# Kernel optimization log

Hardware: AMD Instinct MI355X
Metric: run time of the kernel (lower is better)

The kernel has to match this reference:

```python
import jax, jax.numpy as jnp
import numpy as np

B, T, D, H, L = 64, 256, 64, 512, 10


def setup_inputs() -> dict:
    key = jax.random.key(0)
    ks = jax.random.split(key, 8)
    k_init = 1.0 / np.sqrt(H)  # PyTorch LSTMCell/Linear uniform init bound
    u = lambda k, shape: jax.random.uniform(k, shape, jnp.float32, -k_init, k_init)
    return {
        "x": jax.random.normal(ks[0], (B, T, D), jnp.float32),
        "W_ih0": u(ks[1], (4 * H, D)),        # layer 0 input weights
        "W_ih": u(ks[2], (L - 1, 4 * H, H)),  # layers 1..L-1 input weights
        "W_hh": u(ks[3], (L, 4 * H, H)),      # recurrent weights
        "b_ih": u(ks[4], (L, 4 * H)),
        "b_hh": u(ks[5], (L, 4 * H)),
        "W_out": u(ks[6], (D, H)),            # linear head weight
        "b_out": u(ks[7], (D,)),
    }


def _cell(x, h, c, W_i, W_h, b):
    # PyTorch LSTMCell: gates ordered (i, f, g, o)
    g = x @ W_i.T + h @ W_h.T + b  # [B, 4H]
    i, f, gg, o = jnp.split(g, 4, axis=-1)
    i = jax.nn.sigmoid(i)
    f = jax.nn.sigmoid(f)
    o = jax.nn.sigmoid(o)
    gg = jnp.tanh(gg)
    c_new = f * c + i * gg
    h_new = o * jnp.tanh(c_new)
    return h_new, c_new


def reference(x, W_ih0, W_ih, W_hh, b_ih, b_hh, W_out, b_out):
    b = b_ih + b_hh  # [L, 4H] — biases only ever appear summed

    def step(carry, x_t):
        h, c = carry  # each [L, B, H]
        h0, c0 = _cell(x_t, h[0], c[0], W_ih0, W_hh[0], b[0])
        hs, cs = [h0], [c0]
        for i in range(1, L):  # fixed small layer count
            hi, ci = _cell(hs[-1], h[i], c[i], W_ih[i - 1], W_hh[i], b[i])
            hs.append(hi)
            cs.append(ci)
        y = hs[-1] @ W_out.T + b_out  # [B, D] per-step linear head
        return (jnp.stack(hs), jnp.stack(cs)), y

    init = (jnp.zeros((L, B, H), jnp.float32), jnp.zeros((L, B, H), jnp.float32))
    _, ys = jax.lax.scan(step, init, jnp.swapaxes(x, 0, 1))  # ys: [T, B, D]
    return jnp.swapaxes(ys, 0, 1)  # [B, T, D]
```

## Files before the change

kernel.cpp:

```cpp
#include <hip/hip_runtime.h>
#include <hip/hip_fp16.h>
#include <stdint.h>

typedef _Float16 h8 __attribute__((ext_vector_type(8)));
typedef float f4 __attribute__((ext_vector_type(4)));

#define MFMA16(a,b,c) __builtin_amdgcn_mfma_f32_16x16x32_f16((a),(b),(c),0,0,0)

constexpr size_t XT_OFF = 0;
constexpr size_t XT_BYTES = 256ull * 4096 * 2;
constexpr size_t HL_OFF = XT_OFF + XT_BYTES;
constexpr size_t HL_BYTES = 10ull * 8 * 65536;
constexpr size_t HX_OFF = HL_OFF + HL_BYTES;
constexpr size_t HX_BYTES = 5ull * 8 * 65536;
constexpr size_t WSTRM_OFF = HX_OFF + HX_BYTES;
constexpr size_t WSTRM_BYTES = 144ull * 106496;
constexpr size_t PX_OFF = WSTRM_OFF + WSTRM_BYTES;
constexpr size_t CNT_OFF = PX_OFF + 1024;
constexpr size_t DIAG_OFF = CNT_OFF + 64;
constexpr size_t WS_NEED = DIAG_OFF + 64;

#define SCR 155648

__device__ __forceinline__ const char* unif(const void* p) {
  uint64_t u = (uint64_t)p;
  uint32_t lo = __builtin_amdgcn_readfirstlane((uint32_t)u);
  uint32_t hi = __builtin_amdgcn_readfirstlane((uint32_t)(u >> 32));
  return (const char*)(((uint64_t)hi << 32) | lo);
}

__device__ __forceinline__ h8 gld16_p(const void* base, int voff) {
  h8 v; asm volatile("global_load_dwordx4 %0, %1, %2" : "=v"(v) : "v"(voff), "s"(base)); return v;
}
__device__ __forceinline__ h8 gld16_sc1(const void* base, int voff) {
  h8 v; asm volatile("global_load_dwordx4 %0, %1, %2 sc1" : "=v"(v) : "v"(voff), "s"(base)); return v;
}
__device__ __forceinline__ void gst16_sc1(const void* base, int voff, h8 v) {
  asm volatile("global_store_dwordx4 %0, %1, %2 sc1" :: "v"(voff), "v"(v), "s"(base) : "memory");
}
#define WAITI(n) do { asm volatile("s_waitcnt vmcnt(" #n ")" ::: "memory"); \
                      __builtin_amdgcn_sched_barrier(0); } while (0)

__device__ __forceinline__ int ld_prog(const int* p) {
  return __hip_atomic_load(p, __ATOMIC_RELAXED, __HIP_MEMORY_SCOPE_AGENT);
}
__device__ __forceinline__ void st_prog(int* p, int v) {
  __hip_atomic_store(p, v, __ATOMIC_RELAXED, __HIP_MEMORY_SCOPE_AGENT);
  __builtin_amdgcn_sched_barrier(0);
}
#define INV_L1() asm volatile("buffer_inv sc0\n\ts_waitcnt vmcnt(0)" ::: "memory")

__device__ __forceinline__ float sigm(float x) { return __fdividef(1.f, 1.f + __expf(-x)); }
__device__ __forceinline__ float tanh_f(float x) { return 1.f - __fdividef(2.f, __expf(2.f*x) + 1.f); }

__global__ __launch_bounds__(256) void zero_kernel(char* ws) {
  int i = blockIdx.x * 256 + threadIdx.x;
  if (i < 163840) {
    int layer = i >> 14, w = i & 16383;
    ((int*)(ws + HL_OFF))[(size_t)layer * 8 * 16384 + w] = 0;
  } else {
    int j = i - 163840;
    if (j < 168) ((int*)(ws + PX_OFF))[j] = -1;
    else if (j < 176) ((int*)(ws + CNT_OFF))[j - 168] = 0;
    else if (j == 176) ((int*)(ws + DIAG_OFF))[0] = 0;
  }
}

__global__ __launch_bounds__(256) void xprep_kernel(const float* __restrict__ X, char* ws) {
  int u = blockIdx.x * 256 + threadIdx.x;
  if (u >= 131072) return;
  int t = u >> 9, rem = u & 511, kg = rem >> 6, b = rem & 63;
  const float* src = X + ((size_t)b * 256 + t) * 64 + kg * 8;
  h8 v;
#pragma unroll
  for (int j = 0; j < 8; ++j) v[j] = (_Float16)src[j];
  *(h8*)(ws + XT_OFF + (size_t)u * 16) = v;
}

__global__ __launch_bounds__(256) void wsprep_kernel(const float* __restrict__ Wih,
                                                     const float* __restrict__ Whh, char* ws) {
  int u = blockIdx.x * 256 + threadIdx.x;
  if (u >= 144 * 6656) return;
  int cu = u / 6656, rem = u % 6656;
  int s = rem / 512, rem2 = rem % 512;
  int nt = rem2 >> 6, l = rem2 & 63;
  int ppc = l >> 2, lgc = l & 3;
  int L = 1 + cu / 16, cl = cu % 16, hbase = cl * 32;
  int kt = 4 + s, k = kt * 32 + lgc * 8;
  int row = (nt & 3) * 512 + hbase + ((nt >> 2) << 4) + ppc;
  const float* src = (k < 512) ? (Wih + (size_t)(L - 1) * 1048576 + (size_t)row * 512 + k)
                               : (Whh + (size_t)L * 1048576 + (size_t)row * 512 + (k - 512));
  h8 v;
#pragma unroll
  for (int j = 0; j < 8; ++j) v[j] = (_Float16)src[j];
  uint32_t off = (uint32_t)(ppc * 64 + lgc * 16) ^ (uint32_t)((ppc & 7) << 4);
  *(h8*)(ws + WSTRM_OFF + (size_t)cu * 106496 + (size_t)s * 8192 + (size_t)nt * 1024 + off) = v;
}

#define KTRES(r, Areg) do {                                                     \
  _Pragma("unroll") for (int nt_ = 0; nt_ < 8; ++nt_) {                         \
    h8 bv_ = *(const h8*)(lds + ((((r) * 8 + nt_) << 10) + swzo));              \
    acc[nt_] = MFMA16((Areg), bv_, acc[nt_]); } } while (0)

#define KTSTR(s, Areg) do {                                                     \
  _Pragma("unroll") for (int nt_ = 0; nt_ < 8; ++nt_)                           \
    acc[nt_] = MFMA16((Areg), Bst[s][nt_], acc[nt_]); } while (0)

#define ISSB(s) do { _Pragma("unroll") for (int nt_ = 0; nt_ < 8; ++nt_)        \
    Bst[s][nt_] = gld16_p(strm, (s) * 8192 + (nt_ << 10) + (int)swzo); } while (0)

#define ISSAS(i0) do { _Pragma("unroll") for (int i_ = 0; i_ < 4; ++i_)         \
    AS[(i0) + i_] = gld16_p(selb, ((i0) + i_) * 4096 + abb); } while (0)

__global__ __launch_bounds__(256, 1) void lstm_fused(
    const float* __restrict__ X, const float* __restrict__ Wih0,
    const float* __restrict__ Wih, const float* __restrict__ Whh,
    const float* __restrict__ bih, const float* __restrict__ bhh,
    const float* __restrict__ Wout, const float* __restrict__ bout,
    float* __restrict__ out, char* __restrict__ ws)
{
  extern __shared__ char lds[];
  const int tid = threadIdx.x;
  const int lane = tid & 63;
  const int wv = tid >> 6;
  const int pp = lane & 15;
  const int lg = lane >> 4;
  const int abb = lg * 1024 + (16 * wv + pp) * 16;
  const uint32_t swzo = (uint32_t)(pp * 64 + lg * 16) ^ (uint32_t)((pp & 7) << 4);

  int* progX = (int*)(ws + PX_OFF);
  int* diag  = (int*)(ws + DIAG_OFF);
  const char* hl = ws + HL_OFF;
  const char* hx = ws + HX_OFF;

  int xcd;
  asm volatile("s_getreg_b32 %0, hwreg(HW_REG_XCC_ID)" : "=s"(xcd));
  xcd &= 7;
  if (tid == 0) {
    int s = atomicAdd((int*)(ws + CNT_OFF) + xcd, 1);
    *(int*)lds = s;
  }
  __syncthreads();
  const int slot = __builtin_amdgcn_readfirstlane(*(int*)lds);
  __syncthreads();

  if (xcd == 5) {
    if (slot >= 8) return;
    const int hd = slot, d0 = hd * 8;
    const float* wrow0 = Wout + (size_t)(d0 + wv) * 512;
    const float* wrow1 = Wout + (size_t)(d0 + 4 + wv) * 512;
    const int b = lane;
    const bool pv = lane < 16;
    const int* pw = progX + 144 + (lane & 15);
    for (int th = 0; th < 256; ++th) {
      if (wv == 0) {
        int it = 0; bool bailed = false;
        for (;;) {
          int v = ld_prog(pw);
          if (__ballot(!pv || v >= th) == ~0ull) break;
          __builtin_amdgcn_s_sleep(1);
          if (++it > 60000) { bailed = true; break; }
        }
        if (bailed && lane == 0) atomicMax(diag, 10000 + th);
      }
      __builtin_amdgcn_s_barrier();
      const char* h9 = unif(hx + (size_t)(4 * 8 + ((th + 1) & 7)) * 65536);
      h8 H0[16], H1[16], H2[16], H3[16];
#pragma unroll
      for (int i = 0; i < 16; ++i) H0[i] = gld16_sc1(h9, i * 1024 + b * 16);
#pragma unroll
      for (int i = 0; i < 16; ++i) H1[i] = gld16_sc1(h9, (16 + i) * 1024 + b * 16);
      float a0 = bout[d0 + wv], a1 = bout[d0 + 4 + wv];
#define KH(kb, H) do { _Pragma("unroll") for (int i_ = 0; i_ < 16; ++i_) {      \
        h8 hv_ = H[i_]; float hf_[8];                                           \
        _Pragma("unroll") for (int j_ = 0; j_ < 8; ++j_) hf_[j_] = (float)hv_[j_]; \
        int kg_ = (kb) + i_;                                                    \
        f4 w0_ = *(const f4*)(wrow0 + kg_ * 8); f4 w1_ = *(const f4*)(wrow0 + kg_ * 8 + 4); \
        a0 += hf_[0]*w0_[0]+hf_[1]*w0_[1]+hf_[2]*w0_[2]+hf_[3]*w0_[3]           \
            + hf_[4]*w1_[0]+hf_[5]*w1_[1]+hf_[6]*w1_[2]+hf_[7]*w1_[3];          \
        f4 u0_ = *(const f4*)(wrow1 + kg_ * 8); f4 u1_ = *(const f4*)(wrow1 + kg_ * 8 + 4); \
        a1 += hf_[0]*u0_[0]+hf_[1]*u0_[1]+hf_[2]*u0_[2]+hf_[3]*u0_[3]           \
            + hf_[4]*u1_[0]+hf_[5]*u1_[1]+hf_[6]*u1_[2]+hf_[7]*u1_[3]; } } while (0)
      WAITI(16); KH(0, H0);
#pragma unroll
      for (int i = 0; i < 16; ++i) H2[i] = gld16_sc1(h9, (32 + i) * 1024 + b * 16);
      WAITI(16); KH(16, H1);
#pragma unroll
      for (int i = 0; i < 16; ++i) H3[i] = gld16_sc1(h9, (48 + i) * 1024 + b * 16);
      WAITI(16); KH(32, H2);
      WAITI(0);  KH(48, H3);
      out[(size_t)b * 16384 + (size_t)th * 64 + d0 + wv] = a0;
      out[(size_t)b * 16384 + (size_t)th * 64 + d0 + 4 + wv] = a1;
      __syncthreads();
      if (tid == 0) st_prog(progX + 160 + hd, th);
    }
    if (hd == 0 && tid == 0) {
      int dv = ld_prog(diag);
      if (dv != 0) out[0] = 1.0e6f + (float)dv;
    }
    return;
  }
  if (xcd > 5 || slot >= 32) return;

  const int L = 2 * xcd + (slot >= 16);
  const int cl = slot & 15;
  const int hbase = cl * 32;
  const bool oddL = (L & 1) != 0;

  if (L == 0) {
    for (int ch = tid; ch < 9216; ch += 256) {
      int r = ch >> 9, rem = ch & 511;
      int nt = rem >> 6, l = rem & 63, ppc = l >> 2, lgc = l & 3;
      int k = r * 32 + lgc * 8;
      int row = (nt & 3) * 512 + hbase + ((nt >> 2) << 4) + ppc;
      const float* src = (k < 64) ? (Wih0 + (size_t)row * 64 + k)
                                  : (Whh + (size_t)row * 512 + (k - 64));
      h8 v;
#pragma unroll
      for (int j = 0; j < 8; ++j) v[j] = (_Float16)src[j];
      uint32_t off = (uint32_t)(ppc * 64 + lgc * 16) ^ (uint32_t)((ppc & 7) << 4);
      *(h8*)(lds + ((r * 8 + nt) << 10) + off) = v;
    }
  } else {
    const float* WihL = Wih + (size_t)(L - 1) * 1048576;
    const float* WhhL = Whh + (size_t)L * 1048576;
    for (int ch = tid; ch < 9728; ch += 256) {
      int r = ch >> 9, rem = ch & 511;
      int nt = rem >> 6, l = rem & 63, ppc = l >> 2, lgc = l & 3;
      int rkt = r < 4 ? r : r + 13;
      int k = rkt * 32 + lgc * 8;
      int row = (nt & 3) * 512 + hbase + ((nt >> 2) << 4) + ppc;
      const float* src = (k < 512) ? (WihL + (size_t)row * 512 + k)
                                   : (WhhL + (size_t)row * 512 + (k - 512));
      h8 v;
#pragma unroll
      for (int j = 0; j < 8; ++j) v[j] = (_Float16)src[j];
      uint32_t off = (uint32_t)(ppc * 64 + lgc * 16) ^ (uint32_t)((ppc & 7) << 4);
      *(h8*)(lds + ((r * 8 + nt) << 10) + off) = v;
    }
  }
  float biasv[8];
#pragma unroll
  for (int nt = 0; nt < 8; ++nt) {
    int row = (nt & 3) * 512 + hbase + ((nt >> 2) << 4) + pp;
    biasv[nt] = bih[L * 2048 + row] + bhh[L * 2048 + row];
  }
  __syncthreads();

  const int jl = lane & 15;
  const int* pw = progX; bool pv = false; int dlt = 0;
  if (lane < 16)      { pv = true; pw = progX + L * 16 + jl; dlt = -1; }
  else if (lane < 32) { if (L > 0) { pv = true; pw = progX + (L - 1) * 16 + jl; dlt = 0; } }
  else if (lane < 48) {
    dlt = -7;
    if (L == 9) { if (jl < 8) { pv = true; pw = progX + 160 + jl; } }
    else        { pv = true; pw = progX + (L + 1) * 16 + jl; }
  }

  const char* strm = unif(ws + WSTRM_OFF + (size_t)((L - 1) * 16 + cl) * 106496);
  const char* xt = ws + XT_OFF;

  float cv[2][4] = {{0,0,0,0},{0,0,0,0}};

  for (int t = 0; t < 256; ++t) {
    if (wv == 0) {
      int it = 0; bool bailed = false;
      for (;;) {
        int v = ld_prog(pw);
        if (__ballot(!pv || v >= t + dlt) == ~0ull) break;
        __builtin_amdgcn_s_sleep(1);
        if (++it > 60000) { bailed = true; break; }
      }
      if (bailed && lane == 0) atomicMax(diag, L * 1000 + t);
      INV_L1();
    }
    __builtin_amdgcn_s_barrier();

    f4 acc[8];
#pragma unroll
    for (int j = 0; j < 8; ++j) acc[j] = (f4){0.f, 0.f, 0.f, 0.f};

    if (L == 0) {
      const char* selb = unif(hl + (size_t)(t & 7) * 65536);
      const char* xtb = unif(xt + (size_t)t * 8192);
      h8 X0 = gld16_p(xtb, abb);
      h8 X1 = gld16_p(xtb, 4096 + abb);
      h8 AS[16];
#pragma unroll
      for (int i = 0; i < 16; ++i) AS[i] = gld16_p(selb, i * 4096 + abb);
      WAITI(17); KTRES(0, X0);
      WAITI(16); KTRES(1, X1);
      WAITI(15); KTRES(2, AS[0]);  WAITI(14); KTRES(3, AS[1]);
      WAITI(13); KTRES(4, AS[2]);  WAITI(12); KTRES(5, AS[3]);
      WAITI(11); KTRES(6, AS[4]);  WAITI(10); KTRES(7, AS[5]);
      WAITI(9);  KTRES(8, AS[6]);  WAITI(8);  KTRES(9, AS[7]);
      WAITI(7);  KTRES(10, AS[8]); WAITI(6);  KTRES(11, AS[9]);
      WAITI(5);  KTRES(12, AS[10]); WAITI(4); KTRES(13, AS[11]);
      WAITI(3);  KTRES(14, AS[12]); WAITI(2); KTRES(15, AS[13]);
      WAITI(1);  KTRES(16, AS[14]); WAITI(0); KTRES(17, AS[15]);
    } else {
      const char* botb = unif(oddL
          ? (hl + (size_t)((L - 1) * 8 + ((t + 1) & 7)) * 65536)
          : (hx + (size_t)(((L - 1) >> 1) * 8 + ((t + 1) & 7)) * 65536));
      const char* selb = unif(hl + (size_t)(L * 8 + (t & 7)) * 65536);
      h8 AB[16], AS[16], Bst[13][8];
      if (oddL) {
#pragma unroll
        for (int i = 0; i < 16; ++i) AB[i] = gld16_p(botb, i * 4096 + abb);
      } else {
#pragma unroll
        for (int i = 0; i < 16; ++i) AB[i] = gld16_sc1(botb, i * 4096 + abb);
      }
      ISSB(0); ISSB(1);
      WAITI(31); KTRES(0, AB[0]); ISSB(2);
      WAITI(38); KTRES(1, AB[1]); ISSB(3);
      WAITI(45); KTRES(2, AB[2]); ISSB(4);
      WAITI(52); KTRES(3, AB[3]); ISSB(5);
      WAITI(40); KTSTR(0, AB[4]); ISSB(6);
      WAITI(40); KTSTR(1, AB[5]); ISSB(7);
      WAITI(40); KTSTR(2, AB[6]); ISSB(8);
      WAITI(40); KTSTR(3, AB[7]); ISSB(9);
      WAITI(40); KTSTR(4, AB[8]); ISSB(10);
      WAITI(40); KTSTR(5, AB[9]); ISSB(11);
      WAITI(40); KTSTR(6, AB[10]); ISSB(12);
      WAITI(40); KTSTR(7, AB[11]); ISSAS(0);
      WAITI(36); KTSTR(8, AB[12]); ISSAS(4);
      WAITI(28); KTSTR(9, AB[13]); ISSAS(8);
      WAITI(20); KTSTR(10, AB[14]); ISSAS(12);
      WAITI(12); KTSTR(11, AB[15]);
      WAITI(4);  KTSTR(12, AS[0]);
      KTRES(4, AS[1]);  KTRES(5, AS[2]);  KTRES(6, AS[3]);
      KTRES(7, AS[4]);  KTRES(8, AS[5]);  KTRES(9, AS[6]);
      KTRES(10, AS[7]); KTRES(11, AS[8]); KTRES(12, AS[9]);
      KTRES(13, AS[10]); KTRES(14, AS[11]);
      WAITI(3); KTRES(15, AS[12]);
      WAITI(2); KTRES(16, AS[13]);
      WAITI(1); KTRES(17, AS[14]);
      WAITI(0); KTRES(18, AS[15]);
    }

    const int brow = 16 * wv + 4 * lg;
#pragma unroll
    for (int jh = 0; jh < 2; ++jh) {
      const int hgl = jh * 16 + pp;
#pragma unroll
      for (int r = 0; r < 4; ++r) {
        float gi = sigm(acc[4*jh+0][r] + biasv[4*jh+0]);
        float gf = sigm(acc[4*jh+1][r] + biasv[4*jh+1]);
        float gg = tanh_f(acc[4*jh+2][r] + biasv[4*jh+2]);
        float go = sigm(acc[4*jh+3][r] + biasv[4*jh+3]);
        float cc = gf * cv[jh][r] + gi * gg;
        cv[jh][r] = cc;
        float hh = go * tanh_f(cc);
        *(_Float16*)(lds + SCR + ((hgl >> 3) << 10) + (brow + r) * 16 + ((hgl & 7) << 1))
            = (_Float16)hh;
      }
    }
    __syncthreads();
    {
      const int kg_l = tid >> 6, b = tid & 63;
      h8 vv = *(const h8*)(lds + SCR + tid * 16);
      const int goff = (((hbase >> 3) + kg_l) << 10) + b * 16;
      const char* HdL = unif(hl + (size_t)(L * 8 + ((t + 1) & 7)) * 65536);
      asm volatile("global_store_dwordx4 %0, %1, %2" :: "v"(goff), "v"(vv), "s"(HdL) : "memory");
      if (oddL) {
        const char* HdX = unif(hx + (size_t)((L >> 1) * 8 + ((t + 1) & 7)) * 65536);
        gst16_sc1(HdX, goff, vv);
      }
    }
    asm volatile("s_waitcnt vmcnt(0)" ::: "memory");
    __syncthreads();
    if (tid == 0) st_prog(progX + L * 16 + cl, t);
  }
}

extern "C" void kernel_launch(void* const* d_in, const int* in_sizes, int n_in,
                              void* d_out, int out_size, void* d_ws, size_t ws_size,
                              hipStream_t stream) {
  const float* X    = (const float*)d_in[0];
  const float* Wih0 = (const float*)d_in[1];
  const float* Wih  = (const float*)d_in[2];
  const float* Whh  = (const float*)d_in[3];
  const float* bihp = (const float*)d_in[4];
  const float* bhhp = (const float*)d_in[5];
  const float* Wout = (const float*)d_in[6];
  const float* bout = (const float*)d_in[7];
  float* out = (float*)d_out;
  char* ws = (char*)d_ws;
  (void)in_sizes; (void)n_in; (void)out_size;
  if (ws_size < WS_NEED) return;

  hipFuncSetAttribute((const void*)lstm_fused,
                      hipFuncAttributeMaxDynamicSharedMemorySize, 163840);

  zero_kernel<<<642, 256, 0, stream>>>(ws);
  xprep_kernel<<<512, 256, 0, stream>>>(X, ws);
  wsprep_kernel<<<3744, 256, 0, stream>>>(Wih, Whh, ws);
  lstm_fused<<<256, 256, 163840, stream>>>(X, Wih0, Wih, Whh, bihp, bhhp,
                                           Wout, bout, out, ws);
}
```

Before: 2.912 ms.

## Double waves per block by splitting gate columns across wave pairs

Raises the block size from 256 to 512 threads. Each pair of waves now shares one batch row group and splits the 8 gate column tiles, four per wave, which halves the accumulators, streamed B registers and MFMA chain length per wave. The goal is more latency hiding and a shorter per-step critical path in the serial recurrence. In exchange, both waves of a pair load the same A fragments, block barriers now span more waves, and the vmcnt wait counts and layer-0 LDS indexing had to be retuned by hand.

New measurement: 5.882 ms. +102.0%, slower.

```diff
diff --git a/kernel.cpp b/kernel.cpp
--- a/kernel.cpp
+++ b/kernel.cpp
@@ -34,6 +34,9 @@
 }
 __device__ __forceinline__ h8 gld16_sc1(const void* base, int voff) {
   h8 v; asm volatile("global_load_dwordx4 %0, %1, %2 sc1" : "=v"(v) : "v"(voff), "s"(base)); return v;
+}
+__device__ __forceinline__ void gst16_p(const void* base, int voff, h8 v) {
+  asm volatile("global_store_dwordx4 %0, %1, %2" :: "v"(voff), "v"(v), "s"(base) : "memory");
 }
 __device__ __forceinline__ void gst16_sc1(const void* base, int voff, h8 v) {
   asm volatile("global_store_dwordx4 %0, %1, %2 sc1" :: "v"(voff), "v"(v), "s"(base) : "memory");
@@ -98,21 +101,29 @@
 }
 
 #define KTRES(r, Areg) do {                                                     \
-  _Pragma("unroll") for (int nt_ = 0; nt_ < 8; ++nt_) {                         \
-    h8 bv_ = *(const h8*)(lds + ((((r) * 8 + nt_) << 10) + swzo));              \
+  _Pragma("unroll") for (int nt_ = 0; nt_ < 4; ++nt_) {                         \
+    h8 bv_ = *(const h8*)(lds + ((((r) * 8 + c4 + nt_) << 10) + swzo));         \
     acc[nt_] = MFMA16((Areg), bv_, acc[nt_]); } } while (0)
 
 #define KTSTR(s, Areg) do {                                                     \
-  _Pragma("unroll") for (int nt_ = 0; nt_ < 8; ++nt_)                           \
+  _Pragma("unroll") for (int nt_ = 0; nt_ < 4; ++nt_)                           \
     acc[nt_] = MFMA16((Areg), Bst[s][nt_], acc[nt_]); } while (0)
 
-#define ISSB(s) do { _Pragma("unroll") for (int nt_ = 0; nt_ < 8; ++nt_)        \
-    Bst[s][nt_] = gld16_p(strm, (s) * 8192 + (nt_ << 10) + (int)swzo); } while (0)
+#define ISSB(s) do { _Pragma("unroll") for (int nt_ = 0; nt_ < 4; ++nt_)        \
+    Bst[s][nt_] = gld16_p(strm, (s) * 8192 + ((c4 + nt_) << 10) + (int)swzo); } while (0)
 
 #define ISSAS(i0) do { _Pragma("unroll") for (int i_ = 0; i_ < 4; ++i_)         \
     AS[(i0) + i_] = gld16_p(selb, ((i0) + i_) * 4096 + abb); } while (0)
 
-__global__ __launch_bounds__(256, 1) void lstm_fused(
+#define KB0(kt, Av) do {                                                        \
+  _Pragma("unroll") for (int jj_ = 0; jj_ < 4; ++jj_) {                         \
+    int c_ = 16 * (c4 + jj_) + pp;                                              \
+    uint32_t off_ = (uint32_t)(c_ * 1152 + (kt) * 64 + lg * 16)                 \
+                  ^ (uint32_t)((c_ & 7) << 4);                                  \
+    h8 bv_ = *(const h8*)(lds + off_);                                          \
+    acc[jj_] = MFMA16((Av), bv_, acc[jj_]); } } while (0)
+
+__global__ __launch_bounds__(512, 1) void lstm_fused(
     const float* __restrict__ X, const float* __restrict__ Wih0,
     const float* __restrict__ Wih, const float* __restrict__ Whh,
     const float* __restrict__ bih, const float* __restrict__ bhh,
@@ -123,9 +134,12 @@
   const int tid = threadIdx.x;
   const int lane = tid & 63;
   const int wv = tid >> 6;
+  const int g = wv >> 1;
+  const int cw = wv & 1;
+  const int c4 = cw << 2;
   const int pp = lane & 15;
   const int lg = lane >> 4;
-  const int abb = lg * 1024 + (16 * wv + pp) * 16;
+  const int abb = lg * 1024 + (16 * g + pp) * 16;
   const uint32_t swzo = (uint32_t)(pp * 64 + lg * 16) ^ (uint32_t)((pp & 7) << 4);
 
   int* progX = (int*)(ws + PX_OFF);
@@ -163,14 +177,15 @@
         }
         if (bailed && lane == 0) atomicMax(diag, 10000 + th);
       }
-      __builtin_amdgcn_s_barrier();
-      const char* h9 = unif(hx + (size_t)(4 * 8 + ((th + 1) & 7)) * 65536);
-      h8 H0[16], H1[16], H2[16], H3[16];
-#pragma unroll
-      for (int i = 0; i < 16; ++i) H0[i] = gld16_sc1(h9, i * 1024 + b * 16);
-#pragma unroll
-      for (int i = 0; i < 16; ++i) H1[i] = gld16_sc1(h9, (16 + i) * 1024 + b * 16);
-      float a0 = bout[d0 + wv], a1 = bout[d0 + 4 + wv];
+      __syncthreads();
+      if (wv < 4) {
+        const char* h9 = unif(hx + (size_t)(4 * 8 + ((th + 1) & 7)) * 65536);
+        h8 H0[16], H1[16], H2[16], H3[16];
+#pragma unroll
+        for (int i = 0; i < 16; ++i) H0[i] = gld16_sc1(h9, i * 1024 + b * 16);
+#pragma unroll
+        for (int i = 0; i < 16; ++i) H1[i] = gld16_sc1(h9, (16 + i) * 1024 + b * 16);
+        float a0 = bout[d0 + wv], a1 = bout[d0 + 4 + wv];
 #define KH(kb, H) do { _Pragma("unroll") for (int i_ = 0; i_ < 16; ++i_) {      \
         h8 hv_ = H[i_]; float hf_[8];                                           \
         _Pragma("unroll") for (int j_ = 0; j_ < 8; ++j_) hf_[j_] = (float)hv_[j_]; \
@@ -181,16 +196,17 @@
         f4 u0_ = *(const f4*)(wrow1 + kg_ * 8); f4 u1_ = *(const f4*)(wrow1 + kg_ * 8 + 4); \
         a1 += hf_[0]*u0_[0]+hf_[1]*u0_[1]+hf_[2]*u0_[2]+hf_[3]*u0_[3]           \
             + hf_[4]*u1_[0]+hf_[5]*u1_[1]+hf_[6]*u1_[2]+hf_[7]*u1_[3]; } } while (0)
-      WAITI(16); KH(0, H0);
-#pragma unroll
-      for (int i = 0; i < 16; ++i) H2[i] = gld16_sc1(h9, (32 + i) * 1024 + b * 16);
-      WAITI(16); KH(16, H1);
-#pragma unroll
-      for (int i = 0; i < 16; ++i) H3[i] = gld16_sc1(h9, (48 + i) * 1024 + b * 16);
-      WAITI(16); KH(32, H2);
-      WAITI(0);  KH(48, H3);
-      out[(size_t)b * 16384 + (size_t)th * 64 + d0 + wv] = a0;
-      out[(size_t)b * 16384 + (size_t)th * 64 + d0 + 4 + wv] = a1;
+        WAITI(16); KH(0, H0);
+#pragma unroll
+        for (int i = 0; i < 16; ++i) H2[i] = gld16_sc1(h9, (32 + i) * 1024 + b * 16);
+        WAITI(16); KH(16, H1);
+#pragma unroll
+        for (int i = 0; i < 16; ++i) H3[i] = gld16_sc1(h9, (48 + i) * 1024 + b * 16);
+        WAITI(16); KH(32, H2);
+        WAITI(0);  KH(48, H3);
+        out[(size_t)b * 16384 + (size_t)th * 64 + d0 + wv] = a0;
+        out[(size_t)b * 16384 + (size_t)th * 64 + d0 + 4 + wv] = a1;
+      }
       __syncthreads();
       if (tid == 0) st_prog(progX + 160 + hd, th);
     }
@@ -208,7 +224,7 @@
   const bool oddL = (L & 1) != 0;
 
   if (L == 0) {
-    for (int ch = tid; ch < 9216; ch += 256) {
+    for (int ch = tid; ch < 9216; ch += 512) {
       int r = ch >> 9, rem = ch & 511;
       int nt = rem >> 6, l = rem & 63, ppc = l >> 2, lgc = l & 3;
       int k = r * 32 + lgc * 8;
@@ -224,7 +240,7 @@
   } else {
     const float* WihL = Wih + (size_t)(L - 1) * 1048576;
     const float* WhhL = Whh + (size_t)L * 1048576;
-    for (int ch = tid; ch < 9728; ch += 256) {
+    for (int ch = tid; ch < 9728; ch += 512) {
       int r = ch >> 9, rem = ch & 511;
       int nt = rem >> 6, l = rem & 63, ppc = l >> 2, lgc = l & 3;
       int rkt = r < 4 ? r : r + 13;
@@ -239,11 +255,11 @@
       *(h8*)(lds + ((r * 8 + nt) << 10) + off) = v;
     }
   }
-  float biasv[8];
-#pragma unroll
-  for (int nt = 0; nt < 8; ++nt) {
-    int row = (nt & 3) * 512 + hbase + ((nt >> 2) << 4) + pp;
-    biasv[nt] = bih[L * 2048 + row] + bhh[L * 2048 + row];
+  float biasv[4];
+#pragma unroll
+  for (int j = 0; j < 4; ++j) {
+    int row = j * 512 + hbase + (cw << 4) + pp;
+    biasv[j] = bih[L * 2048 + row] + bhh[L * 2048 + row];
   }
   __syncthreads();
 
@@ -260,7 +276,7 @@
   const char* strm = unif(ws + WSTRM_OFF + (size_t)((L - 1) * 16 + cl) * 106496);
   const char* xt = ws + XT_OFF;
 
-  float cv[2][4] = {{0,0,0,0},{0,0,0,0}};
+  float cv[4] = {0,0,0,0};
 
   for (int t = 0; t < 256; ++t) {
     if (wv == 0) {
@@ -274,11 +290,11 @@
       if (bailed && lane == 0) atomicMax(diag, L * 1000 + t);
       INV_L1();
     }
-    __builtin_amdgcn_s_barrier();
-
-    f4 acc[8];
-#pragma unroll
-    for (int j = 0; j < 8; ++j) acc[j] = (f4){0.f, 0.f, 0.f, 0.f};
+    __syncthreads();
+
+    f4 acc[4];
+#pragma unroll
+    for (int j = 0; j < 4; ++j) acc[j] = (f4){0.f, 0.f, 0.f, 0.f};
 
     if (L == 0) {
       const char* selb = unif(hl + (size_t)(t & 7) * 65536);
@@ -288,22 +304,22 @@
       h8 AS[16];
 #pragma unroll
       for (int i = 0; i < 16; ++i) AS[i] = gld16_p(selb, i * 4096 + abb);
-      WAITI(17); KTRES(0, X0);
-      WAITI(16); KTRES(1, X1);
-      WAITI(15); KTRES(2, AS[0]);  WAITI(14); KTRES(3, AS[1]);
-      WAITI(13); KTRES(4, AS[2]);  WAITI(12); KTRES(5, AS[3]);
-      WAITI(11); KTRES(6, AS[4]);  WAITI(10); KTRES(7, AS[5]);
-      WAITI(9);  KTRES(8, AS[6]);  WAITI(8);  KTRES(9, AS[7]);
-      WAITI(7);  KTRES(10, AS[8]); WAITI(6);  KTRES(11, AS[9]);
-      WAITI(5);  KTRES(12, AS[10]); WAITI(4); KTRES(13, AS[11]);
-      WAITI(3);  KTRES(14, AS[12]); WAITI(2); KTRES(15, AS[13]);
-      WAITI(1);  KTRES(16, AS[14]); WAITI(0); KTRES(17, AS[15]);
+      WAITI(17); KB0(0, X0);
+      WAITI(16); KB0(1, X1);
+      WAITI(15); KB0(2, AS[0]);  WAITI(14); KB0(3, AS[1]);
+      WAITI(13); KB0(4, AS[2]);  WAITI(12); KB0(5, AS[3]);
+      WAITI(11); KB0(6, AS[4]);  WAITI(10); KB0(7, AS[5]);
+      WAITI(9);  KB0(8, AS[6]);  WAITI(8);  KB0(9, AS[7]);
+      WAITI(7);  KB0(10, AS[8]); WAITI(6);  KB0(11, AS[9]);
+      WAITI(5);  KB0(12, AS[10]); WAITI(4); KB0(13, AS[11]);
+      WAITI(3);  KB0(14, AS[12]); WAITI(2); KB0(15, AS[13]);
+      WAITI(1);  KB0(16, AS[14]); WAITI(0); KB0(17, AS[15]);
     } else {
       const char* botb = unif(oddL
           ? (hl + (size_t)((L - 1) * 8 + ((t + 1) & 7)) * 65536)
           : (hx + (size_t)(((L - 1) >> 1) * 8 + ((t + 1) & 7)) * 65536));
       const char* selb = unif(hl + (size_t)(L * 8 + (t & 7)) * 65536);
-      h8 AB[16], AS[16], Bst[13][8];
+      h8 AB[16], AS[16], Bst[13][4];
       if (oddL) {
 #pragma unroll
         for (int i = 0; i < 16; ++i) AB[i] = gld16_p(botb, i * 4096 + abb);
@@ -312,57 +328,61 @@
         for (int i = 0; i < 16; ++i) AB[i] = gld16_sc1(botb, i * 4096 + abb);
       }
       ISSB(0); ISSB(1);
-      WAITI(31); KTRES(0, AB[0]); ISSB(2);
-      WAITI(38); KTRES(1, AB[1]); ISSB(3);
-      WAITI(45); KTRES(2, AB[2]); ISSB(4);
-      WAITI(52); KTRES(3, AB[3]); ISSB(5);
-      WAITI(40); KTSTR(0, AB[4]); ISSB(6);
-      WAITI(40); KTSTR(1, AB[5]); ISSB(7);
-      WAITI(40); KTSTR(2, AB[6]); ISSB(8);
-      WAITI(40); KTSTR(3, AB[7]); ISSB(9);
-      WAITI(40); KTSTR(4, AB[8]); ISSB(10);
-      WAITI(40); KTSTR(5, AB[9]); ISSB(11);
-      WAITI(40); KTSTR(6, AB[10]); ISSB(12);
-      WAITI(40); KTSTR(7, AB[11]); ISSAS(0);
-      WAITI(36); KTSTR(8, AB[12]); ISSAS(4);
-      WAITI(28); KTSTR(9, AB[13]); ISSAS(8);
+      WAITI(23); KTRES(0, AB[0]); ISSB(2);
+      WAITI(26); KTRES(1, AB[1]); ISSB(3);
+      WAITI(29); KTRES(2, AB[2]); ISSB(4);
+      WAITI(32); KTRES(3, AB[3]); ISSB(5);
+      WAITI(20); KTSTR(0, AB[4]); ISSB(6);
+      WAITI(20); KTSTR(1, AB[5]); ISSB(7);
+      WAITI(20); KTSTR(2, AB[6]); ISSB(8);
+      WAITI(20); KTSTR(3, AB[7]); ISSB(9);
+      WAITI(20); KTSTR(4, AB[8]); ISSB(10);
+      WAITI(20); KTSTR(5, AB[9]); ISSB(11);
+      WAITI(20); KTSTR(6, AB[10]); ISSB(12);
+      WAITI(20); KTSTR(7, AB[11]); ISSAS(0);
+      WAITI(20); KTSTR(8, AB[12]); ISSAS(4);
+      WAITI(20); KTSTR(9, AB[13]); ISSAS(8);
       WAITI(20); KTSTR(10, AB[14]); ISSAS(12);
-      WAITI(12); KTSTR(11, AB[15]);
-      WAITI(4);  KTSTR(12, AS[0]);
-      KTRES(4, AS[1]);  KTRES(5, AS[2]);  KTRES(6, AS[3]);
-      KTRES(7, AS[4]);  KTRES(8, AS[5]);  KTRES(9, AS[6]);
-      KTRES(10, AS[7]); KTRES(11, AS[8]); KTRES(12, AS[9]);
-      KTRES(13, AS[10]); KTRES(14, AS[11]);
-      WAITI(3); KTRES(15, AS[12]);
-      WAITI(2); KTRES(16, AS[13]);
-      WAITI(1); KTRES(17, AS[14]);
-      WAITI(0); KTRES(18, AS[15]);
-    }
-
-    const int brow = 16 * wv + 4 * lg;
-#pragma unroll
-    for (int jh = 0; jh < 2; ++jh) {
-      const int hgl = jh * 16 + pp;
-#pragma unroll
-      for (int r = 0; r < 4; ++r) {
-        float gi = sigm(acc[4*jh+0][r] + biasv[4*jh+0]);
-        float gf = sigm(acc[4*jh+1][r] + biasv[4*jh+1]);
-        float gg = tanh_f(acc[4*jh+2][r] + biasv[4*jh+2]);
-        float go = sigm(acc[4*jh+3][r] + biasv[4*jh+3]);
-        float cc = gf * cv[jh][r] + gi * gg;
-        cv[jh][r] = cc;
-        float hh = go * tanh_f(cc);
-        *(_Float16*)(lds + SCR + ((hgl >> 3) << 10) + (brow + r) * 16 + ((hgl & 7) << 1))
-            = (_Float16)hh;
-      }
+      WAITI(20); KTSTR(11, AB[15]);
+      WAITI(15); KTSTR(12, AS[0]);
+      WAITI(14); KTRES(4, AS[1]);
+      WAITI(13); KTRES(5, AS[2]);
+      WAITI(12); KTRES(6, AS[3]);
+      WAITI(11); KTRES(7, AS[4]);
+      WAITI(10); KTRES(8, AS[5]);
+      WAITI(9);  KTRES(9, AS[6]);
+      WAITI(8);  KTRES(10, AS[7]);
+      WAITI(7);  KTRES(11, AS[8]);
+      WAITI(6);  KTRES(12, AS[9]);
+      WAITI(5);  KTRES(13, AS[10]);
+      WAITI(4);  KTRES(14, AS[11]);
+      WAITI(3);  KTRES(15, AS[12]);
+      WAITI(2);  KTRES(16, AS[13]);
+      WAITI(1);  KTRES(17, AS[14]);
+      WAITI(0);  KTRES(18, AS[15]);
+    }
+
+    const int brow = 16 * g + 4 * lg;
+    const int hgl = 16 * cw + pp;
+#pragma unroll
+    for (int r = 0; r < 4; ++r) {
+      float gi = sigm(acc[0][r] + biasv[0]);
+      float gf = sigm(acc[1][r] + biasv[1]);
+      float gg = tanh_f(acc[2][r] + biasv[2]);
+      float go = sigm(acc[3][r] + biasv[3]);
+      float cc = gf * cv[r] + gi * gg;
+      cv[r] = cc;
+      float hh = go * tanh_f(cc);
+      *(_Float16*)(lds + SCR + ((hgl >> 3) << 10) + (brow + r) * 16 + ((hgl & 7) << 1))
+          = (_Float16)hh;
     }
     __syncthreads();
-    {
+    if (wv < 4) {
       const int kg_l = tid >> 6, b = tid & 63;
       h8 vv = *(const h8*)(lds + SCR + tid * 16);
       const int goff = (((hbase >> 3) + kg_l) << 10) + b * 16;
       const char* HdL = unif(hl + (size_t)(L * 8 + ((t + 1) & 7)) * 65536);
-      asm volatile("global_store_dwordx4 %0, %1, %2" :: "v"(goff), "v"(vv), "s"(HdL) : "memory");
+      gst16_p(HdL, goff, vv);
       if (oddL) {
         const char* HdX = unif(hx + (size_t)((L >> 1) * 8 + ((t + 1) & 7)) * 65536);
         gst16_sc1(HdX, goff, vv);
@@ -396,6 +416,6 @@
   zero_kernel<<<642, 256, 0, stream>>>(ws);
   xprep_kernel<<<512, 256, 0, stream>>>(X, ws);
   wsprep_kernel<<<3744, 256, 0, stream>>>(Wih, Whh, ws);
-  lstm_fused<<<256, 256, 163840, stream>>>(X, Wih0, Wih, Whh, bihp, bhhp,
+  lstm_fused<<<256, 512, 163840, stream>>>(X, Wih0, Wih, Whh, bihp, bhhp,
                                            Wout, bout, out, ws);
 }
```
